# Kernel optimization log

Measured on AMD Instinct MI355X. Metric: run time of the kernel, lower is better.

The kernel has to match this reference:

```python
import jax, jax.numpy as jnp
import numpy as np

EPS = 1e-9
TAU = 100.0
HX = 1.0
HY = 1.0


def _sym_pad(x):
    # torch Pad(1, padding_mode='symmetric') == numpy/jnp 'symmetric'
    return jnp.pad(x, ((0, 0), (0, 0), (1, 1), (1, 1)), mode='symmetric')


def _zero_interior(x):
    # zeroPadGS: keep interior, zero 1-px border
    return jnp.pad(x[:, :, 1:-1, 1:-1], ((0, 0), (0, 0), (1, 1), (1, 1)))


def _frob(x):
    # per-(batch,channel) Frobenius norm; only used in control-flow comparisons
    return jax.lax.stop_gradient(jnp.sqrt(jnp.sum(x * x, axis=(2, 3))))


def _apply_stencil(inp, boo, bmo, bom, bop, bpo):
    # applyStencilGS: mirror-pad interior, apply 5-point stencil, zero border
    p = _sym_pad(inp[:, :, 1:-1, 1:-1])
    res = (boo * p[:, :, 1:-1, 1:-1]
           + bmo * p[:, :, :-2, 1:-1]
           + bom * p[:, :, 1:-1, :-2]
           + bop * p[:, :, 1:-1, 2:]
           + bpo * p[:, :, 2:, 1:-1])
    return jnp.pad(res, ((0, 0), (0, 0), (1, 1), (1, 1)))


def _forward(V, mask1, mask2, kmax):
    B, C, nx0, ny0 = V.shape
    # U = per-image mean of V
    U = jnp.broadcast_to(jnp.mean(V, axis=(2, 3), keepdims=True), V.shape)
    Ut = jnp.swapaxes(_sym_pad(U), 2, 3)
    Vt = jnp.swapaxes(_sym_pad(V), 2, 3)
    m1 = jnp.swapaxes(_sym_pad(mask1), 2, 3)
    m2 = jnp.swapaxes(_sym_pad(mask2), 2, 3)
    nx, ny = ny0, nx0
    # drift vectors: forward difference / forward average (conv f1/f2, f3/f4)
    d1 = (Vt[:, :, 1:, :] - Vt[:, :, :-1, :]) / (HX * 0.5 * (Vt[:, :, 1:, :] + Vt[:, :, :-1, :]))
    d2 = (Vt[:, :, :, 1:] - Vt[:, :, :, :-1]) / (HY * 0.5 * (Vt[:, :, :, 1:] + Vt[:, :, :, :-1]))
    d1f = jnp.zeros_like(Vt).at[:, :, :nx + 1, 1:ny + 1].set(d1[:, :, :, 1:ny + 1]) * m1
    d2f = jnp.zeros_like(Vt).at[:, :, 1:nx + 1, :ny + 1].set(d2[:, :, 1:nx + 1, :]) * m2
    rx, ry = TAU / (2 * HX), TAU / (2 * HY)
    rxx, ryy = TAU / (HX * HX), TAU / (HY * HY)
    # conv 'same' with kernel [1,-1,0] (cross-correlation): out[i] = d[i-1] - d[i]
    c1 = jnp.pad(d1f, ((0, 0), (0, 0), (1, 0), (0, 0)))[:, :, :-1, :] - d1f
    c2 = jnp.pad(d2f, ((0, 0), (0, 0), (0, 0), (1, 0)))[:, :, :, :-1] - d2f
    boo_full = 1 + 2 * (rxx + ryy) - rx * c1 - ry * c2
    boo = boo_full[:, :, 1:nx + 1, 1:ny + 1]
    bpo = -rxx + rx * d1f[:, :, 1:nx + 1, 1:ny + 1]
    bop = -ryy + ry * d2f[:, :, 1:nx + 1, 1:ny + 1]
    bmo = -rxx - rx * d1f[:, :, :nx, 1:ny + 1]
    bom = -ryy - ry * d2f[:, :, 1:nx + 1, :ny]

    A = lambda z: _apply_stencil(z, boo, bmo, bom, bop, bpo)
    thresh = EPS * nx * ny
    x0 = Ut
    b = Ut
    p0 = _zero_interior(b - A(x0))
    r0_abs = _frob(p0)
    zc = jnp.zeros((B, C), dtype=V.dtype)
    zf = jnp.zeros_like(x0)
    k0 = jnp.zeros((B, C), dtype=jnp.int32)
    carry0 = (x0, p0, p0, zf, p0, zf, zf, zf, r0_abs, r0_abs, zc, zc, zc, zc, zc, k0)

    def step(carry, _):
        x, r, r_0, r_old, p, v, s, t, r_abs, r0_abs, sigma, alpha, omega, beta, v_abs, k = carry
        conv = (k < kmax) & (r_abs > thresh)
        convE = conv[:, :, None, None]
        v = jnp.where(convE, A(p), v)
        sigma = jnp.where(conv, jnp.sum(v * r_0, axis=(2, 3)), sigma)
        v_abs = jnp.where(conv, _frob(v), v_abs)
        res = sigma <= EPS * v_abs * r0_abs
        res1 = conv & res
        res1E = res1[:, :, None, None]
        p = jnp.where(res1E, _zero_interior(b - A(x)), p)
        r = jnp.where(res1E, p, r)
        r_0 = jnp.where(res1E, p, r_0)
        r0_abs = jnp.where(res1, _frob(r_0), r0_abs)
        r_abs = jnp.where(res1, r0_abs, r_abs)
        k = jnp.where(res1, k + 1, k)
        nres = conv & ~res
        nresE = nres[:, :, None, None]
        alpha = jnp.where(nres, jnp.sum(r * r_0, axis=(2, 3)) / jnp.where(nres, sigma, 1.0), alpha)
        s = jnp.where(nresE, r - alpha[:, :, None, None] * v, s)
        conv2 = _frob(s) <= thresh
        c3E = (nres & conv2)[:, :, None, None]
        x = jnp.where(c3E, x + alpha[:, :, None, None] * p, x)
        r = jnp.where(c3E, s, r)
        c4 = nres & ~conv2
        c4E = c4[:, :, None, None]
        t = jnp.where(c4E, A(s), t)
        omega = jnp.where(c4, jnp.sum(t * s, axis=(2, 3)) / jnp.where(c4, jnp.sum(t * t, axis=(2, 3)), 1.0), omega)
        x = jnp.where(c4E, x + alpha[:, :, None, None] * p + omega[:, :, None, None] * s, x)
        r_old = jnp.where(c4E, r, r_old)
        r = jnp.where(c4E, s - omega[:, :, None, None] * t, r)
        beta = jnp.where(c4, (alpha / jnp.where(c4, omega, 1.0)) * (jnp.sum(r * r_0, axis=(2, 3)) / jnp.where(c4, jnp.sum(r_old * r_0, axis=(2, 3)), 1.0)), beta)
        p = jnp.where(c4E, r + beta[:, :, None, None] * (p - omega[:, :, None, None] * v), p)
        k = jnp.where(nres, k + 1, k)
        r_abs = jnp.where(nres, _frob(r), r_abs)
        return (x, r, r_0, r_old, p, v, s, t, r_abs, r0_abs, sigma, alpha, omega, beta, v_abs, k), None

    carry, _ = jax.lax.scan(step, carry0, jnp.arange(kmax))
    return carry[0]


def setup_inputs() -> dict:
    key = jax.random.key(0)
    k1, k2, k3 = jax.random.split(key, 3)
    B, C, N = 8, 1, 512
    # strictly positive guidance image (V + offset in the original)
    V = jax.random.uniform(k1, (B, C, N, N), dtype=jnp.float32) * 0.99 + 0.005
    mask1 = (jax.random.uniform(k2, (B, C, N, N)) < 0.1).astype(jnp.float32)
    mask2 = (jax.random.uniform(k3, (B, C, N, N)) < 0.1).astype(jnp.float32)
    return {"V": V, "mask1": mask1, "mask2": mask2, "kmax": 16}


def reference(V, mask1, mask2, kmax):
    return _forward(V, mask1, mask2, kmax)
```

## Files before the change

### kernel.cpp

```cpp
#include <hip/hip_runtime.h>
#include <math.h>


namespace {

typedef unsigned long long ull;

constexpr int NIMG = 8;
constexpr int NSd  = 512;
constexpr int S    = NSd*NSd;
constexpr int NSF  = NIMG*S;
constexpr int PADS = 514;
constexpr int NB   = 256;
constexpr int IPB  = 32;
constexpr int NT   = 512;
constexpr float EPSF = 1e-9f;
constexpr float THR  = 1e-9f * 262144.0f;
constexpr float RX_=50.f, RY_=50.f, RXX_=100.f, RYY_=100.f;
constexpr float BOO0 = 1.f + 2.f*(RXX_+RYY_);

enum { P_PH=0, P_VH, P_TH, NPLH };
constexpr size_t A_QW = (size_t)NIMG*2*8*32;
constexpr size_t B_QW = (size_t)NIMG*2*8;

__device__ __forceinline__ int cl(int i){ return i<0?0:(i>NSd-1?NSd-1:i); }

#define LD4(d, p) { float4 _t4 = *reinterpret_cast<const float4*>(p); \
  (d)[0]=_t4.x; (d)[1]=_t4.y; (d)[2]=_t4.z; (d)[3]=_t4.w; }
#define ST4(p, s) { *reinterpret_cast<float4*>(p) = \
  make_float4((s)[0],(s)[1],(s)[2],(s)[3]); }
#define CP4(d, s) { (d)[0]=(s)[0]; (d)[1]=(s)[1]; (d)[2]=(s)[2]; (d)[3]=(s)[3]; }

#define LOADCOEF(rr_) \
  float ax[4], by[4], bym[4], axl; \
  LD4(ax, &axp[rr_][c4o]); \
  LD4(by, &byp[rr_][c4o]); \
  axl = __shfl_up(ax[3], 1); \
  if (lane==0) axl = c4o ? axp[rr_][c4o-1] : 0.f; \
  if ((rr_) > 0){ LD4(bym, &byp[(rr_)-1][c4o]); } else { CP4(bym, bym0_); }

__device__ __forceinline__ void hstore4(ull* pq, int off_f, const float s[4]){
  size_t q = (size_t)off_f >> 1;
  ull u0 = ((ull)__float_as_uint(s[1])<<32) | (ull)__float_as_uint(s[0]);
  ull u1 = ((ull)__float_as_uint(s[3])<<32) | (ull)__float_as_uint(s[2]);
  __hip_atomic_store(pq+q,   u0, __ATOMIC_RELAXED, __HIP_MEMORY_SCOPE_AGENT);
  __hip_atomic_store(pq+q+1, u1, __ATOMIC_RELAXED, __HIP_MEMORY_SCOPE_AGENT);
}
__device__ __forceinline__ void hload4(const ull* pq, int off_f, float d[4]){
  size_t q = (size_t)off_f >> 1;
  ull u0 = __hip_atomic_load(pq+q,   __ATOMIC_RELAXED, __HIP_MEMORY_SCOPE_AGENT);
  ull u1 = __hip_atomic_load(pq+q+1, __ATOMIC_RELAXED, __HIP_MEMORY_SCOPE_AGENT);
  d[0]=__uint_as_float((unsigned)u0); d[1]=__uint_as_float((unsigned)(u0>>32));
  d[2]=__uint_as_float((unsigned)u1); d[3]=__uint_as_float((unsigned)(u1>>32));
}

__device__ __forceinline__ void phase_sync(ull* Aq, ull* Bq, int img, int sub,
    unsigned ep, float* v, int n){
  __shared__ float acc[8][5];
  __shared__ float bc[5];
  const int tid = threadIdx.x, w = tid>>6, lane = tid&63;
  #pragma unroll
  for (int i=0;i<5;++i){
    if (i<n){
      float a = v[i];
      #pragma unroll
      for (int o=32;o;o>>=1) a += __shfl_xor(a,o);
      if (lane==0) acc[w][i] = a;
    }
  }
  __syncthreads();
  const int par = ep & 1;
  ull* Ab = Aq + ((size_t)(img*2+par)*8)*32;
  ull* Bb = Bq + ((size_t)(img*2+par))*8;
  if (sub == 0){
    if (w < n){
      float own = 0.f;
      #pragma unroll
      for (int i=0;i<8;++i) own += acc[i][w];
      ull x = 0; const bool me = (lane>=1 && lane<32);
      for(;;){
        bool ok = true;
        if (me){
          x = __hip_atomic_load(Ab + w*32 + lane, __ATOMIC_RELAXED, __HIP_MEMORY_SCOPE_AGENT);
          ok = ((unsigned)x == ep);
        }
        if (__all(ok)) break;
        __builtin_amdgcn_s_sleep(1);
      }
      float a = me ? __uint_as_float((unsigned)(x>>32)) : ((lane==0)? own : 0.f);
      #pragma unroll
      for (int o=16;o;o>>=1) a += __shfl_xor(a,o);
      if (lane==0){
        bc[w] = a;
        ull pk = ((ull)__float_as_uint(a)<<32) | (ull)ep;
        __hip_atomic_store(Bb + w, pk, __ATOMIC_RELAXED, __HIP_MEMORY_SCOPE_AGENT);
      }
    }
  } else {
    if (tid < n){
      float t = 0.f;
      #pragma unroll
      for (int i=0;i<8;++i) t += acc[i][tid];
      ull pk = ((ull)__float_as_uint(t)<<32) | (ull)ep;
      __hip_atomic_store(Ab + tid*32 + sub, pk, __ATOMIC_RELAXED, __HIP_MEMORY_SCOPE_AGENT);
    }
    if (w == 0){
      ull x = 0; const bool me = (lane < n);
      for(;;){
        bool ok = true;
        if (me){
          x = __hip_atomic_load(Bb + lane, __ATOMIC_RELAXED, __HIP_MEMORY_SCOPE_AGENT);
          ok = ((unsigned)x == ep);
        }
        if (__all(ok)) break;
        __builtin_amdgcn_s_sleep(1);
      }
      if (me) bc[lane] = __uint_as_float((unsigned)(x>>32));
    }
  }
  __syncthreads();
  #pragma unroll
  for (int i=0;i<5;++i) if (i<n) v[i] = bc[i];
}

__device__ __forceinline__ void stencil_reg(const float zc[4], float zl, float zr,
    const float zu[4], const float zd[4],
    const float ax[4], float axl, const float by[4], const float bym[4],
    float out[4]){
  #pragma unroll
  for (int j=0;j<4;++j){
    float axm = j ? ax[j-1] : axl;
    float zxm = j ? zc[j-1] : zl;
    float zxp = (j<3) ? zc[j+1] : zr;
    float boo = BOO0 + ax[j] - axm + by[j] - bym[j];
    out[j] = boo*zc[j] + (-RXX_-axm)*zxm + (-RYY_-bym[j])*zu[j]
           + (-RYY_+by[j])*zd[j] + (-RXX_+ax[j])*zxp;
  }
}

__global__ void __launch_bounds__(NT)
solve(const float* __restrict__ Vg,
    const float* __restrict__ M1g, const float* __restrict__ M2g,
    const int* __restrict__ kmp, float* __restrict__ outg, float* __restrict__ ws){
  __shared__ float tile[18][NSd];
  __shared__ float r0l[16][NSd];
  __shared__ float axp[16][NSd];
  __shared__ float byp[16][NSd];
  const int tid = threadIdx.x, blk = blockIdx.x;
  const int img = blk & 7, sub = blk >> 3;
  const int y0 = sub*16, bS = img*S;
  const int cg = tid & 127, r0b = tid >> 7, c4o = cg*4;
  const int lane = tid & 63;
  ull* PHq = (ull*)(ws + (size_t)P_PH*NSF);
  ull* VHq = (ull*)(ws + (size_t)P_VH*NSF);
  ull* THq = (ull*)(ws + (size_t)P_TH*NSF);
  ull* Aq  = (ull*)(ws + (size_t)NPLH*NSF);
  ull* Bq  = Aq + A_QW;
  unsigned ep = 0;
  const int kmax = kmp[0];
  const int row0o  = bS + (y0<<9) + c4o;
  const int row15o = bS + ((y0+15)<<9) + c4o;
  const int rowm1o = bS + ((y0-1)<<9) + c4o;
  const int row16o = bS + ((y0+16)<<9) + c4o;
  float red[5];

  float bym0_[4];
  float msum = 0.f;
  #pragma unroll
  for (int k=0;k<4;++k){
    int rr = 4*r0b + k, fy = y0 + rr, ro = bS + (fy<<9);
    float vc[4], vd[4], m1[4], m2[4], ca[4], cb[4];
    LD4(vc, Vg+ro+c4o);
    float vr  = Vg[ro + (c4o<508 ? c4o+4 : 511)];
    LD4(vd, Vg + bS + (cl(fy+1)<<9) + c4o);
    LD4(m1, M1g+ro+c4o);
    LD4(m2, M2g+ro+c4o);
    #pragma unroll
    for (int j=0;j<4;++j){
      float vn = (j<3) ? vc[j+1] : vr;
      ca[j] = RX_*((vn-vc[j])/(0.5f*(vn+vc[j])))*m1[j];
      cb[j] = RY_*((vd[j]-vc[j])/(0.5f*(vd[j]+vc[j])))*m2[j];
      msum += vc[j];
    }
    ST4(&axp[rr][c4o], ca);
    ST4(&byp[rr][c4o], cb);
  }
  if (r0b==0 && sub>0){
    int ro = bS + (y0<<9);
    float vc[4], vu[4], m2u[4];
    LD4(vc, Vg+ro+c4o);
    LD4(vu, Vg + bS + ((y0-1)<<9) + c4o);
    LD4(m2u, M2g + bS + ((y0-1)<<9) + c4o);
    #pragma unroll
    for (int j=0;j<4;++j)
      bym0_[j] = RY_*((vc[j]-vu[j])/(0.5f*(vc[j]+vu[j])))*m2u[j];
  } else {
    bym0_[0]=0.f; bym0_[1]=0.f; bym0_[2]=0.f; bym0_[3]=0.f;
  }
  red[0]=msum;
  ++ep; phase_sync(Aq,Bq,img,sub,ep, red, 1);
  const float c = red[0]*(1.0f/262144.0f);

  float x_[4][4], p_[4][4], r_[4][4], v_[4][4];
  float ph_[4], rh_[4], xh_[4], vh_[4];
  {
    float pa = 0.f;
    #pragma unroll
    for (int k=0;k<4;++k){
      int rr = 4*r0b + k;
      LOADCOEF(rr);
      float pn4[4];
      #pragma unroll
      for (int j=0;j<4;++j){
        float axm = j ? ax[j-1] : axl;
        float pn = -2.f*c*(ax[j]-axm + by[j]-bym[j]);
        x_[k][j]=c; p_[k][j]=pn; r_[k][j]=pn; v_[k][j]=0.f;
        pn4[j]=pn;
        pa += pn*pn;
      }
      ST4(&r0l[rr][c4o], pn4);
    }
    #pragma unroll
    for (int j=0;j<4;++j){ xh_[j]=c; ph_[j]=0.f; rh_[j]=0.f; vh_[j]=0.f; }
    if (r0b==0) hstore4(PHq, row0o, p_[0]);
    if (r0b==3) hstore4(PHq, row15o, p_[3]);
    red[0]=pa;
    ++ep; phase_sync(Aq,Bq,img,sub,ep, red, 1);
  }
  float rr0 = red[0];
  float r0abs = sqrtf(rr0), rabs = r0abs;
  int kcnt = 0;
  bool c4p = false;
  float alpha=0.f, omega=0.f, beta=0.f;

  for (int it=0; it<kmax; ++it){
    if (!((kcnt < kmax) && (rabs > THR))) break;

    if (c4p){
      #pragma unroll
      for (int k=0;k<4;++k)
        #pragma unroll
        for (int j=0;j<4;++j)
          p_[k][j] = r_[k][j] + beta*(p_[k][j]-omega*v_[k][j]);
      if (r0b==0 || r0b==3){
        #pragma unroll
        for (int j=0;j<4;++j) ph_[j] = rh_[j] + beta*(ph_[j]-omega*vh_[j]);
      }
    } else {
      if (r0b==0){
        if (sub==0){ CP4(ph_, p_[0]); } else hload4(PHq, rowm1o, ph_);
        CP4(rh_, ph_);
      }
      if (r0b==3){
        if (sub==IPB-1){ CP4(ph_, p_[3]); } else hload4(PHq, row16o, ph_);
        CP4(rh_, ph_);
      }
    }
    #pragma unroll
    for (int k=0;k<4;++k){ ST4(&tile[4*r0b+k+1][c4o], p_[k]); }
    if (r0b==0) ST4(&tile[0][c4o], ph_);
    if (r0b==3) ST4(&tile[17][c4o], ph_);
    __syncthreads();
    {
      float s1=0.f, s2=0.f;
      #pragma unroll
      for (int k=0;k<4;++k){
        int rr = 4*r0b+k, st = rr+1;
        LOADCOEF(rr);
        float zu[4], zd[4], ov[4], r0v[4];
        LD4(zu, &tile[st-1][c4o]);
        LD4(zd, &tile[st+1][c4o]);
        LD4(r0v, &r0l[rr][c4o]);
        float zl = __shfl_up(p_[k][3], 1);
        float zr = __shfl_down(p_[k][0], 1);
        if (lane==0)  zl = (c4o==0)   ? p_[k][0] : tile[st][c4o-1];
        if (lane==63) zr = (c4o==508) ? p_[k][3] : tile[st][c4o+4];
        stencil_reg(p_[k], zl, zr, zu, zd, ax, axl, by, bym, ov);
        #pragma unroll
        for (int j=0;j<4;++j){
          v_[k][j]=ov[j]; s1 += ov[j]*r0v[j]; s2 += ov[j]*ov[j];
        }
      }
      if (r0b==0) hstore4(VHq, row0o, v_[0]);
      if (r0b==3) hstore4(VHq, row15o, v_[3]);
      red[0]=s1; red[1]=s2;
      ++ep; phase_sync(Aq,Bq,img,sub,ep, red, 2);
    }
    float sig = red[0], vabs = sqrtf(red[1]);

    if (sig <= EPSF*vabs*r0abs){
      #pragma unroll
      for (int k=0;k<4;++k){ ST4(&tile[4*r0b+k+1][c4o], x_[k]); }
      if (r0b==0) ST4(&tile[0][c4o], xh_);
      if (r0b==3) ST4(&tile[17][c4o], xh_);
      __syncthreads();
      float pa = 0.f;
      #pragma unroll
      for (int k=0;k<4;++k){
        int rr = 4*r0b+k, st = rr+1;
        LOADCOEF(rr);
        float zu[4], zd[4], av[4], pn4[4];
        LD4(zu, &tile[st-1][c4o]);
        LD4(zd, &tile[st+1][c4o]);
        float zl = __shfl_up(x_[k][3], 1);
        float zr = __shfl_down(x_[k][0], 1);
        if (lane==0)  zl = (c4o==0)   ? x_[k][0] : tile[st][c4o-1];
        if (lane==63) zr = (c4o==508) ? x_[k][3] : tile[st][c4o+4];
        stencil_reg(x_[k], zl, zr, zu, zd, ax, axl, by, bym, av);
        #pragma unroll
        for (int j=0;j<4;++j){
          float pn = c - av[j];
          p_[k][j]=pn; r_[k][j]=pn; pn4[j]=pn;
          pa += pn*pn;
        }
        ST4(&r0l[rr][c4o], pn4);
      }
      if (r0b==0) hstore4(PHq, row0o, p_[0]);
      if (r0b==3) hstore4(PHq, row15o, p_[3]);
      red[0]=pa;
      ++ep; phase_sync(Aq,Bq,img,sub,ep, red, 1);
      rr0 = red[0]; r0abs = sqrtf(rr0); rabs = r0abs; kcnt++;
      c4p = false;
      continue;
    }

    alpha = rr0 / sig;
    if (r0b==0){
      if (sub==0){ CP4(vh_, v_[0]); } else hload4(VHq, rowm1o, vh_);
    }
    if (r0b==3){
      if (sub==IPB-1){ CP4(vh_, v_[3]); } else hload4(VHq, row16o, vh_);
    }
    float tk[4][4];
    {
      float ssp = 0.f;
      #pragma unroll
      for (int k=0;k<4;++k){
        float sv[4];
        #pragma unroll
        for (int j=0;j<4;++j){
          sv[j] = r_[k][j] - alpha*v_[k][j];
          ssp += sv[j]*sv[j];
        }
        ST4(&tile[4*r0b+k+1][c4o], sv);
      }
      if (r0b==0){
        float sh[4];
        #pragma unroll
        for (int j=0;j<4;++j) sh[j] = rh_[j] - alpha*vh_[j];
        ST4(&tile[0][c4o], sh);
      }
      if (r0b==3){
        float sh[4];
        #pragma unroll
        for (int j=0;j<4;++j) sh[j] = rh_[j] - alpha*vh_[j];
        ST4(&tile[17][c4o], sh);
      }
      __syncthreads();
      float tsp=0.f, ttp=0.f, sr0p=0.f, tr0p=0.f;
      #pragma unroll
      for (int k=0;k<4;++k){
        int rr = 4*r0b+k, st = rr+1;
        LOADCOEF(rr);
        float zc[4], zu[4], zd[4], tv[4], r0v[4];
        #pragma unroll
        for (int j=0;j<4;++j) zc[j] = r_[k][j] - alpha*v_[k][j];
        LD4(zu, &tile[st-1][c4o]);
        LD4(zd, &tile[st+1][c4o]);
        LD4(r0v, &r0l[rr][c4o]);
        float zl = __shfl_up(zc[3], 1);
        float zr = __shfl_down(zc[0], 1);
        if (lane==0)  zl = (c4o==0)   ? zc[0] : tile[st][c4o-1];
        if (lane==63) zr = (c4o==508) ? zc[3] : tile[st][c4o+4];
        stencil_reg(zc, zl, zr, zu, zd, ax, axl, by, bym, tv);
        #pragma unroll
        for (int j=0;j<4;++j){
          tsp  += tv[j]*zc[j];
          ttp  += tv[j]*tv[j];
          sr0p += zc[j]*r0v[j];
          tr0p += tv[j]*r0v[j];
        }
        CP4(tk[k], tv);
      }
      if (r0b==0) hstore4(THq, row0o, tk[0]);
      if (r0b==3) hstore4(THq, row15o, tk[3]);
      __syncthreads();
      #pragma unroll
      for (int k=0;k<4;++k){ ST4(&tile[4*r0b+k+1][c4o], tk[k]); }
      red[0]=ssp; red[1]=tsp; red[2]=ttp; red[3]=sr0p; red[4]=tr0p;
      ++ep; phase_sync(Aq,Bq,img,sub,ep, red, 5);
    }
    float ss=red[0], ts=red[1], tt=red[2], s_r0=red[3], t_r0=red[4];
    float snorm = sqrtf(ss);

    if (snorm <= THR){
      #pragma unroll
      for (int k=0;k<4;++k)
        #pragma unroll
        for (int j=0;j<4;++j) x_[k][j] += alpha*p_[k][j];
      rabs = snorm; kcnt++; c4p = false;
      continue;
    }

    omega = ts/tt;
    #pragma unroll
    for (int k=0;k<4;++k){
      int st = 4*r0b+k+1;
      float tv[4];
      LD4(tv, &tile[st][c4o]);
      #pragma unroll
      for (int j=0;j<4;++j){
        float sv = r_[k][j] - alpha*v_[k][j];
        x_[k][j] = x_[k][j] + alpha*p_[k][j] + omega*sv;
        r_[k][j] = sv - omega*tv[j];
      }
    }
    if (r0b==0){
      float th[4];
      if (sub==0){ CP4(th, tk[0]); } else hload4(THq, rowm1o, th);
      #pragma unroll
      for (int j=0;j<4;++j){
        float sh = rh_[j] - alpha*vh_[j];
        xh_[j] = xh_[j] + alpha*ph_[j] + omega*sh;
        rh_[j] = sh - omega*th[j];
      }
    }
    if (r0b==3){
      float th[4];
      if (sub==IPB-1){ CP4(th, tk[3]); } else hload4(THq, row16o, th);
      #pragma unroll
      for (int j=0;j<4;++j){
        float sh = rh_[j] - alpha*vh_[j];
        xh_[j] = xh_[j] + alpha*ph_[j] + omega*sh;
        rh_[j] = sh - omega*th[j];
      }
    }
    float rr0n = s_r0 - omega*t_r0;
    rabs = sqrtf(fmaxf(ss - 2.f*omega*ts + omega*omega*tt, 0.f));
    beta = alpha/omega*(rr0n/rr0);
    rr0 = rr0n; kcnt++;
    c4p = true;
  }

  __syncthreads();
  float* lp = &tile[0][0];
  #pragma unroll
  for (int k=0;k<4;++k){
    int ri = 4*r0b + k;
    ST4(lp + ri*516 + c4o, x_[k]);
  }
  float* outb = outg + (size_t)img*PADS*PADS;
  if (sub == 0){
    for (int e = tid; e < 2052; e += NT){
      int i, j;
      if (e < 514)      { i=0;        j=e;      }
      else if (e < 1028){ i=513;      j=e-514;  }
      else if (e < 1540){ i=e-1028+1; j=0;      }
      else              { i=e-1540+1; j=513;    }
      outb[i*PADS+j] = c;
    }
  }
  __syncthreads();
  {
    int qq = tid & 15, xb = tid >> 4;
    #pragma unroll
    for (int ps=0; ps<16; ++ps){
      int xc = ps*32 + xb;
      outb[(size_t)(xc+1)*PADS + (y0+1+qq)] = lp[qq*516 + xc];
    }
  }
}

}

extern "C" void kernel_launch(void* const* d_in, const int* in_sizes, int n_in,
                              void* d_out, int out_size, void* d_ws, size_t ws_size,
                              hipStream_t stream){
  const float* V  = (const float*)d_in[0];
  const float* M1 = (const float*)d_in[1];
  const float* M2 = (const float*)d_in[2];
  const int*   km = (const int*)d_in[3];
  float* ws  = (float*)d_ws;
  float* out = (float*)d_out;

  size_t need = (size_t)NPLH*NSF*sizeof(float) + (A_QW + B_QW)*sizeof(ull);
  if (ws_size < need) return;

  hipMemsetAsync((char*)d_ws + (size_t)NPLH*NSF*sizeof(float),
                 0, (A_QW + B_QW)*sizeof(ull), stream);

  solve<<<dim3(NB), dim3(NT), 0, stream>>>(V, M1, M2, km, out, ws);
}
```

Measured before the change: 210.7 us.

## Merge initial reductions into one sync and compute halo rows locally

The initial mean and the residual-norm reduction are fused into a single cross-block sync, using the identity that the initial residual norm is 4c²·Σg². Halo rows of the initial search direction are recomputed from global V and the masks instead of being exchanged through global memory. Halo reload now happens only after a restart. phase_sync also drops s_sleep backoff and has every wave poll the broadcast slot itself rather than one wave followed by __syncthreads. This removes one grid-wide barrier plus a halo exchange, at the cost of more polling traffic and extra global loads for the halo rows.

```diff
diff --git a/kernel.cpp b/kernel.cpp
--- a/kernel.cpp
+++ b/kernel.cpp
@@ -54,10 +54,36 @@
   d[2]=__uint_as_float((unsigned)u1); d[3]=__uint_as_float((unsigned)(u1>>32));
 }
 
+__device__ __forceinline__ void g_row_global(const float* __restrict__ Vg,
+    const float* __restrict__ M1g, const float* __restrict__ M2g,
+    int bS, int fy, int c4o, float gh[4]){
+  int ro = bS + (fy<<9);
+  float vc[4], vd[4], m1[4], m2[4], vu[4], m2u[4];
+  LD4(vc, Vg+ro+c4o);
+  float vr  = Vg[ro + (c4o<508 ? c4o+4 : 511)];
+  float vl  = c4o ? Vg[ro+c4o-1]  : vc[0];
+  float m1l = c4o ? M1g[ro+c4o-1] : 0.f;
+  LD4(vd, Vg + bS + (cl(fy+1)<<9) + c4o);
+  LD4(m1, M1g+ro+c4o);
+  LD4(m2, M2g+ro+c4o);
+  bool up = (fy > 0);
+  if (up){ LD4(vu, Vg + bS + ((fy-1)<<9) + c4o); LD4(m2u, M2g + bS + ((fy-1)<<9) + c4o); }
+  else { vu[0]=vu[1]=vu[2]=vu[3]=0.f; m2u[0]=m2u[1]=m2u[2]=m2u[3]=0.f; }
+  float axm = c4o ? RX_*((vc[0]-vl)/(0.5f*(vc[0]+vl)))*m1l : 0.f;
+  #pragma unroll
+  for (int j=0;j<4;++j){
+    float vn = (j<3) ? vc[j+1] : vr;
+    float axj  = RX_*((vn-vc[j])/(0.5f*(vn+vc[j])))*m1[j];
+    float byj  = RY_*((vd[j]-vc[j])/(0.5f*(vd[j]+vc[j])))*m2[j];
+    float bymj = up ? RY_*((vc[j]-vu[j])/(0.5f*(vc[j]+vu[j])))*m2u[j] : 0.f;
+    gh[j] = axj - axm + byj - bymj;
+    axm = axj;
+  }
+}
+
 __device__ __forceinline__ void phase_sync(ull* Aq, ull* Bq, int img, int sub,
     unsigned ep, float* v, int n){
   __shared__ float acc[8][5];
-  __shared__ float bc[5];
   const int tid = threadIdx.x, w = tid>>6, lane = tid&63;
   #pragma unroll
   for (int i=0;i<5;++i){
@@ -85,13 +111,11 @@
           ok = ((unsigned)x == ep);
         }
         if (__all(ok)) break;
-        __builtin_amdgcn_s_sleep(1);
       }
       float a = me ? __uint_as_float((unsigned)(x>>32)) : ((lane==0)? own : 0.f);
       #pragma unroll
       for (int o=16;o;o>>=1) a += __shfl_xor(a,o);
       if (lane==0){
-        bc[w] = a;
         ull pk = ((ull)__float_as_uint(a)<<32) | (ull)ep;
         __hip_atomic_store(Bb + w, pk, __ATOMIC_RELAXED, __HIP_MEMORY_SCOPE_AGENT);
       }
@@ -104,23 +128,21 @@
       ull pk = ((ull)__float_as_uint(t)<<32) | (ull)ep;
       __hip_atomic_store(Ab + tid*32 + sub, pk, __ATOMIC_RELAXED, __HIP_MEMORY_SCOPE_AGENT);
     }
-    if (w == 0){
-      ull x = 0; const bool me = (lane < n);
-      for(;;){
-        bool ok = true;
-        if (me){
-          x = __hip_atomic_load(Bb + lane, __ATOMIC_RELAXED, __HIP_MEMORY_SCOPE_AGENT);
-          ok = ((unsigned)x == ep);
-        }
-        if (__all(ok)) break;
-        __builtin_amdgcn_s_sleep(1);
-      }
-      if (me) bc[lane] = __uint_as_float((unsigned)(x>>32));
-    }
-  }
-  __syncthreads();
-  #pragma unroll
-  for (int i=0;i<5;++i) if (i<n) v[i] = bc[i];
+  }
+  {
+    ull x = 0; const bool me = (lane < n);
+    for(;;){
+      bool ok = true;
+      if (me){
+        x = __hip_atomic_load(Bb + lane, __ATOMIC_RELAXED, __HIP_MEMORY_SCOPE_AGENT);
+        ok = ((unsigned)x == ep);
+      }
+      if (__all(ok)) break;
+    }
+    float val = me ? __uint_as_float((unsigned)(x>>32)) : 0.f;
+    #pragma unroll
+    for (int i=0;i<5;++i) if (i<n) v[i] = __shfl(val, i);
+  }
 }
 
 __device__ __forceinline__ void stencil_reg(const float zc[4], float zl, float zr,
@@ -197,40 +219,65 @@
   } else {
     bym0_[0]=0.f; bym0_[1]=0.f; bym0_[2]=0.f; bym0_[3]=0.f;
   }
-  red[0]=msum;
-  ++ep; phase_sync(Aq,Bq,img,sub,ep, red, 1);
-  const float c = red[0]*(1.0f/262144.0f);
-
-  float x_[4][4], p_[4][4], r_[4][4], v_[4][4];
-  float ph_[4], rh_[4], xh_[4], vh_[4];
+  __syncthreads();
   {
-    float pa = 0.f;
+    float ggs = 0.f;
     #pragma unroll
     for (int k=0;k<4;++k){
       int rr = 4*r0b + k;
       LOADCOEF(rr);
-      float pn4[4];
       #pragma unroll
       for (int j=0;j<4;++j){
         float axm = j ? ax[j-1] : axl;
-        float pn = -2.f*c*(ax[j]-axm + by[j]-bym[j]);
-        x_[k][j]=c; p_[k][j]=pn; r_[k][j]=pn; v_[k][j]=0.f;
-        pn4[j]=pn;
-        pa += pn*pn;
-      }
-      ST4(&r0l[rr][c4o], pn4);
-    }
-    #pragma unroll
-    for (int j=0;j<4;++j){ xh_[j]=c; ph_[j]=0.f; rh_[j]=0.f; vh_[j]=0.f; }
-    if (r0b==0) hstore4(PHq, row0o, p_[0]);
-    if (r0b==3) hstore4(PHq, row15o, p_[3]);
-    red[0]=pa;
-    ++ep; phase_sync(Aq,Bq,img,sub,ep, red, 1);
-  }
-  float rr0 = red[0];
+        float g = ax[j]-axm + by[j]-bym[j];
+        ggs += g*g;
+      }
+    }
+    red[0]=msum; red[1]=ggs;
+  }
+  ++ep; phase_sync(Aq,Bq,img,sub,ep, red, 2);
+  const float c = red[0]*(1.0f/262144.0f);
+  float rr0 = 4.f*c*c*red[1];
   float r0abs = sqrtf(rr0), rabs = r0abs;
+
+  float x_[4][4], p_[4][4], r_[4][4], v_[4][4];
+  float ph_[4], rh_[4], xh_[4], vh_[4];
+  #pragma unroll
+  for (int k=0;k<4;++k){
+    int rr = 4*r0b + k;
+    LOADCOEF(rr);
+    float pn4[4];
+    #pragma unroll
+    for (int j=0;j<4;++j){
+      float axm = j ? ax[j-1] : axl;
+      float pn = -2.f*c*(ax[j]-axm + by[j]-bym[j]);
+      x_[k][j]=c; p_[k][j]=pn; r_[k][j]=pn; v_[k][j]=0.f;
+      pn4[j]=pn;
+    }
+    ST4(&r0l[rr][c4o], pn4);
+  }
+  #pragma unroll
+  for (int j=0;j<4;++j){ xh_[j]=c; ph_[j]=0.f; rh_[j]=0.f; vh_[j]=0.f; }
+  if (r0b==0){
+    if (sub==0){ CP4(ph_, p_[0]); }
+    else {
+      float gh[4]; g_row_global(Vg,M1g,M2g,bS,y0-1,c4o,gh);
+      #pragma unroll
+      for (int j=0;j<4;++j) ph_[j] = -2.f*c*gh[j];
+    }
+    CP4(rh_, ph_);
+  }
+  if (r0b==3){
+    if (sub==IPB-1){ CP4(ph_, p_[3]); }
+    else {
+      float gh[4]; g_row_global(Vg,M1g,M2g,bS,y0+16,c4o,gh);
+      #pragma unroll
+      for (int j=0;j<4;++j) ph_[j] = -2.f*c*gh[j];
+    }
+    CP4(rh_, ph_);
+  }
   int kcnt = 0;
-  bool c4p = false;
+  bool c4p = false, need_refresh = false;
   float alpha=0.f, omega=0.f, beta=0.f;
 
   for (int it=0; it<kmax; ++it){
@@ -246,7 +293,7 @@
         #pragma unroll
         for (int j=0;j<4;++j) ph_[j] = rh_[j] + beta*(ph_[j]-omega*vh_[j]);
       }
-    } else {
+    } else if (need_refresh){
       if (r0b==0){
         if (sub==0){ CP4(ph_, p_[0]); } else hload4(PHq, rowm1o, ph_);
         CP4(rh_, ph_);
@@ -255,6 +302,7 @@
         if (sub==IPB-1){ CP4(ph_, p_[3]); } else hload4(PHq, row16o, ph_);
         CP4(rh_, ph_);
       }
+      need_refresh = false;
     }
     #pragma unroll
     for (int k=0;k<4;++k){ ST4(&tile[4*r0b+k+1][c4o], p_[k]); }
@@ -320,7 +368,7 @@
       red[0]=pa;
       ++ep; phase_sync(Aq,Bq,img,sub,ep, red, 1);
       rr0 = red[0]; r0abs = sqrtf(rr0); rabs = r0abs; kcnt++;
-      c4p = false;
+      c4p = false; need_refresh = true;
       continue;
     }
 
```

Result: slower. 263.0 us (+24.8%).
